# Kernel tuning notes

Hardware: AMD Instinct MI355X
Metric: run time of the kernel (lower is better)

The kernel has to match this reference:

```python
import jax, jax.numpy as jnp
import numpy as np

B, L, D = 2, 4096, 128      # batch, seq_len, d_model
ED = 2 * D                  # d_inner (expand=2) = 256
N = 16                      # d_state
K = 4                       # d_conv
R = (D + 15) // 16          # dt_rank = 8
H = 2 * D                   # mlp hidden = 256


def setup_inputs() -> dict:
    key = jax.random.key(0)
    ks = jax.random.split(key, 20)
    s = 0.05
    inp = {
        "x": jax.random.normal(ks[0], (B, L, D), dtype=jnp.float32),
        # outer block LayerNorm (norm1)
        "norm1_g": jnp.ones((D,), jnp.float32),
        "norm1_b": jnp.zeros((D,), jnp.float32),
        # MambaLayer inner LayerNorm
        "inner_g": jnp.ones((D,), jnp.float32),
        "inner_b": jnp.zeros((D,), jnp.float32),
        # Mamba params
        "in_w": jax.random.normal(ks[1], (2 * ED, D), jnp.float32) * s,      # in_proj (no bias)
        "conv_w": jax.random.normal(ks[2], (ED, 1, K), jnp.float32) * s,     # depthwise conv
        "conv_b": jax.random.normal(ks[3], (ED,), jnp.float32) * s,
        "xproj_w": jax.random.normal(ks[4], (R + 2 * N, ED), jnp.float32) * s,  # x_proj (no bias)
        "dt_w": jax.random.normal(ks[5], (ED, R), jnp.float32) * s,
        "dt_b": jax.random.normal(ks[6], (ED,), jnp.float32) * s,
        "A_log": jnp.tile(jnp.log(jnp.arange(1, N + 1, dtype=jnp.float32)), (ED, 1)),  # [ED,N]
        "Dp": jnp.ones((ED,), jnp.float32),
        "out_w": jax.random.normal(ks[7], (D, ED), jnp.float32) * s,         # out_proj (no bias)
        # MLP
        "fc1_w": jax.random.normal(ks[8], (H, D), jnp.float32) * s,
        "fc1_b": jnp.zeros((H,), jnp.float32),
        "fc2_w": jax.random.normal(ks[9], (D, H), jnp.float32) * s,
        "fc2_b": jnp.zeros((D,), jnp.float32),
    }
    return inp


def _ln(x, g, b, eps=1e-5):
    m = jnp.mean(x, axis=-1, keepdims=True)
    v = jnp.mean((x - m) ** 2, axis=-1, keepdims=True)
    return (x - m) * jax.lax.rsqrt(v + eps) * g + b


def _mamba(x, in_w, conv_w, conv_b, xproj_w, dt_w, dt_b, A_log, Dp, out_w):
    # x: [B, L, D]
    xz = jnp.einsum('bld,ed->ble', x, in_w)          # [B,L,2*ED]
    u, z = jnp.split(xz, 2, axis=-1)                 # each [B,L,ED]
    # causal depthwise conv1d over L
    u_c = jnp.transpose(u, (0, 2, 1))                # [B,ED,L]
    u_c = jax.lax.conv_general_dilated(
        u_c, conv_w, window_strides=(1,), padding=[(K - 1, 0)],
        dimension_numbers=('NCH', 'OIH', 'NCH'), feature_group_count=ED)
    u = jax.nn.silu(jnp.transpose(u_c, (0, 2, 1)) + conv_b)   # [B,L,ED]
    # input-dependent dt, B, C
    dbc = jnp.einsum('ble,re->blr', u, xproj_w)      # [B,L,R+2N]
    dt, Bm, Cm = jnp.split(dbc, [R, R + N], axis=-1)
    delta = jax.nn.softplus(jnp.einsum('blr,er->ble', dt, dt_w) + dt_b)  # [B,L,ED]
    A = -jnp.exp(A_log)                              # [ED,N]
    deltaA = jnp.exp(jnp.einsum('ble,en->blen', delta, A))               # [B,L,ED,N]
    deltaBu = jnp.einsum('ble,bln,ble->blen', delta, Bm, u)              # [B,L,ED,N]
    # selective scan over L
    def step(h, inp):
        dA, dBu, Ct = inp                            # [B,ED,N],[B,ED,N],[B,N]
        h = dA * h + dBu
        y = jnp.einsum('ben,bn->be', h, Ct)
        return h, y
    h0 = jnp.zeros((B, ED, N), u.dtype)
    xs = (jnp.transpose(deltaA, (1, 0, 2, 3)),
          jnp.transpose(deltaBu, (1, 0, 2, 3)),
          jnp.transpose(Cm, (1, 0, 2)))
    _, ys = jax.lax.scan(step, h0, xs)               # [L,B,ED]
    y = jnp.transpose(ys, (1, 0, 2)) + u * Dp        # [B,L,ED]
    y = y * jax.nn.silu(z)
    return jnp.einsum('ble,de->bld', y, out_w)       # [B,L,D]


def reference(x, norm1_g, norm1_b, inner_g, inner_b, in_w, conv_w, conv_b,
              xproj_w, dt_w, dt_b, A_log, Dp, out_w, fc1_w, fc1_b, fc2_w, fc2_b):
    # attn branch: mamba(inner_LN(norm1(x)))
    a = _mamba(_ln(_ln(x, norm1_g, norm1_b), inner_g, inner_b),
               in_w, conv_w, conv_b, xproj_w, dt_w, dt_b, A_log, Dp, out_w)
    x = x + a
    # mlp branch (note: original applies norm1 again to updated x)
    h = _ln(x, norm1_g, norm1_b)
    h = jax.nn.gelu(jnp.einsum('bld,hd->blh', h, fc1_w) + fc1_b, approximate=False)
    h = jnp.einsum('blh,dh->bld', h, fc2_w) + fc2_b
    return x + h
```

## Files before the change

kernel.cpp:

```cpp
#include <hip/hip_runtime.h>
#include <hip/hip_bf16.h>
#include <math.h>

#define BB 2
#define LL 4096
#define DD 128
#define ED 256
#define NN 16
#define KK 4
#define RR 8
#define HH 256
#define NT (BB*LL)
#define NC 128
#define LC 32
#define NCS 256
#define LCS 16

#define LOG2E 1.4426950408889634f

typedef __attribute__((ext_vector_type(8))) short short8;
typedef __attribute__((ext_vector_type(8))) unsigned short ushort8v;
typedef __attribute__((ext_vector_type(4))) float floatx4;

__device__ __forceinline__ unsigned short f2bf(float f) {
  unsigned int b = __builtin_bit_cast(unsigned int, f);
  b += 0x7FFFu + ((b >> 16) & 1u);
  return (unsigned short)(b >> 16);
}

__device__ __forceinline__ float exp2_fast(float x) {
#if __has_builtin(__builtin_amdgcn_exp2f)
  return __builtin_amdgcn_exp2f(x);
#else
  return exp2f(x);
#endif
}

__device__ __forceinline__ ushort8v pack8(const float4& v0, const float4& v1) {
  ushort8v p;
  p[0]=f2bf(v0.x); p[1]=f2bf(v0.y); p[2]=f2bf(v0.z); p[3]=f2bf(v0.w);
  p[4]=f2bf(v1.x); p[5]=f2bf(v1.y); p[6]=f2bf(v1.z); p[7]=f2bf(v1.w);
  return p;
}

__global__ __launch_bounds__(512, 4) void scan1j_k(
    const float* __restrict__ x,
    const float* __restrict__ g1, const float* __restrict__ b1,
    const float* __restrict__ g2, const float* __restrict__ b2,
    const float* __restrict__ in_w,
    const float* __restrict__ cw, const float* __restrict__ cb,
    const float* __restrict__ xpw,
    const float* __restrict__ dtw, const float* __restrict__ dtb,
    const float* __restrict__ A_log,
    float* __restrict__ uc, float* __restrict__ dbc,
    float* __restrict__ delta, float* __restrict__ gate,
    float* __restrict__ cA, float* __restrict__ cH) {
  __shared__ __align__(16) unsigned char SM[51152];
  auto Atile = reinterpret_cast<unsigned short(*)[136]>(SM);
  auto As    = reinterpret_cast<unsigned short(*)[264]>(SM);
  auto Wch   = reinterpret_cast<unsigned short(*)[136]>(SM + 8704);
  auto Bs    = reinterpret_cast<unsigned short(*)[264]>(SM + 8704);
  auto ubuf  = reinterpret_cast<float(*)[65]>(SM + 29824);
  auto sdbc  = reinterpret_cast<float(*)[40]>(SM + 29824);
  auto sus   = reinterpret_cast<float(*)[256]>(SM + 34768);

  const int c2 = blockIdx.x, b = blockIdx.y;
  const int tid = threadIdx.x;
  const int t0 = b*LL + c2*LCS;
  const int wave = tid >> 6, lane = tid & 63;
  const int quad = lane >> 4, l16 = lane & 15;

  {
    const int lr = tid >> 2, lk = (tid & 3) * 32;
    if (lr < 32) {
      if (lr < 19 && !(c2 == 0 && lr < 3)) {
        const float* Ap = x + (size_t)(t0 - 3 + lr)*DD + lk;
        float4 av[8];
        float s = 0.f, sq = 0.f;
        #pragma unroll
        for (int g = 0; g < 8; g++) {
          av[g] = *(const float4*)(Ap + g*4);
          s  += av[g].x + av[g].y + av[g].z + av[g].w;
          sq += av[g].x*av[g].x + av[g].y*av[g].y + av[g].z*av[g].z + av[g].w*av[g].w;
        }
        s += __shfl_xor(s, 1);  s += __shfl_xor(s, 2);
        sq += __shfl_xor(sq, 1); sq += __shfl_xor(sq, 2);
        const float m1 = s * (1.f/128.f);
        const float rs1 = rsqrtf(sq*(1.f/128.f) - m1*m1 + 1e-5f);
        float s2 = 0.f, sq2 = 0.f;
        #pragma unroll
        for (int g = 0; g < 8; g++) {
          const float4 gg = *(const float4*)(g1 + lk + g*4);
          const float4 bb = *(const float4*)(b1 + lk + g*4);
          av[g].x = (av[g].x - m1)*rs1*gg.x + bb.x;
          av[g].y = (av[g].y - m1)*rs1*gg.y + bb.y;
          av[g].z = (av[g].z - m1)*rs1*gg.z + bb.z;
          av[g].w = (av[g].w - m1)*rs1*gg.w + bb.w;
          s2  += av[g].x + av[g].y + av[g].z + av[g].w;
          sq2 += av[g].x*av[g].x + av[g].y*av[g].y + av[g].z*av[g].z + av[g].w*av[g].w;
        }
        s2 += __shfl_xor(s2, 1);  s2 += __shfl_xor(s2, 2);
        sq2 += __shfl_xor(sq2, 1); sq2 += __shfl_xor(sq2, 2);
        const float m2 = s2 * (1.f/128.f);
        const float rs2 = rsqrtf(sq2*(1.f/128.f) - m2*m2 + 1e-5f);
        #pragma unroll
        for (int g = 0; g < 4; g++) {
          const float4 ga = *(const float4*)(g2 + lk + g*8);
          const float4 gb = *(const float4*)(g2 + lk + g*8 + 4);
          const float4 ba = *(const float4*)(b2 + lk + g*8);
          const float4 bbv= *(const float4*)(b2 + lk + g*8 + 4);
          ushort8v pa;
          pa[0] = f2bf((av[2*g].x   - m2)*rs2*ga.x + ba.x);
          pa[1] = f2bf((av[2*g].y   - m2)*rs2*ga.y + ba.y);
          pa[2] = f2bf((av[2*g].z   - m2)*rs2*ga.z + ba.z);
          pa[3] = f2bf((av[2*g].w   - m2)*rs2*ga.w + ba.w);
          pa[4] = f2bf((av[2*g+1].x - m2)*rs2*gb.x + bbv.x);
          pa[5] = f2bf((av[2*g+1].y - m2)*rs2*gb.y + bbv.y);
          pa[6] = f2bf((av[2*g+1].z - m2)*rs2*gb.z + bbv.z);
          pa[7] = f2bf((av[2*g+1].w - m2)*rs2*gb.w + bbv.w);
          *(ushort8v*)&Atile[lr][lk + g*8] = pa;
        }
      } else {
        const ushort8v zz = {};
        #pragma unroll
        for (int g = 0; g < 4; g++) *(ushort8v*)&Atile[lr][lk + g*8] = zz;
      }
    }
  }
  __syncthreads();

  short8 af[2][4];
  #pragma unroll
  for (int mt = 0; mt < 2; mt++)
    #pragma unroll
    for (int ks = 0; ks < 4; ks++)
      af[mt][ks] = *(const short8*)&Atile[mt*16 + l16][ks*32 + quad*8];

  {
    const int wr = tid >> 3;
    const int wseg = (tid & 7) * 16;
    const int mt_w = wave & 1, nt_w = wave >> 1;
    float4 wv[4];
    #pragma unroll
    for (int g = 0; g < 4; g++)
      wv[g] = *(const float4*)(in_w + (size_t)wr*DD + wseg + g*4);
    for (int nc = 0; nc < 8; nc++) {
      *(ushort8v*)&Wch[wr][wseg]     = pack8(wv[0], wv[1]);
      *(ushort8v*)&Wch[wr][wseg + 8] = pack8(wv[2], wv[3]);
      __syncthreads();
      if (nc < 7) {
        const float* wp = in_w + (size_t)((nc+1)*64 + wr)*DD + wseg;
        #pragma unroll
        for (int g = 0; g < 4; g++) wv[g] = *(const float4*)(wp + g*4);
      }
      floatx4 acc = {};
      #pragma unroll
      for (int ks = 0; ks < 4; ks++) {
        short8 bv = *(const short8*)&Wch[nt_w*16 + l16][ks*32 + quad*8];
        acc = __builtin_amdgcn_mfma_f32_16x16x32_bf16(af[mt_w][ks], bv, acc, 0, 0, 0);
      }
      const int coll = nt_w*16 + l16;
      if (nc < 4) {
        #pragma unroll
        for (int rr = 0; rr < 4; rr++) {
          const int m = mt_w*16 + quad*4 + rr;
          if (m < 19) ubuf[m][coll] = acc[rr];
        }
      } else {
        const int gcol = (nc-4)*64 + coll;
        #pragma unroll
        for (int rr = 0; rr < 4; rr++) {
          const int m = mt_w*16 + quad*4 + rr;
          if (m >= 3 && m < 19) {
            const float v = acc[rr];
            gate[(size_t)(t0 + m - 3)*ED + gcol] = v / (1.f + __expf(-v));
          }
        }
      }
      __syncthreads();
      if (nc < 4) {
        const int chl = tid & 63, tg = tid >> 6;
        const int ch = nc*64 + chl;
        const float4 w = *(const float4*)(cw + ch*4);
        const float cbe = cb[ch];
        const int i0 = tg*2;
        float v0 = ubuf[i0][chl], v1 = ubuf[i0+1][chl], v2 = ubuf[i0+2][chl];
        #pragma unroll
        for (int k = 0; k < 2; k++) {
          const float cur = ubuf[i0+3+k][chl];
          const float a = cbe + v0*w.x + v1*w.y + v2*w.z + cur*w.w;
          const float s = a / (1.f + __expf(-a));
          const int i = i0 + k;
          As[i][ch] = f2bf(s);
          sus[i][ch] = s;
          uc[(size_t)(t0+i)*ED + ch] = s;
          v0 = v1; v1 = v2; v2 = cur;
        }
      }
    }
  }
  __syncthreads();

  #pragma unroll
  for (int p = 0; p < 3; p++) {
    const int idx = p*512 + tid;
    if (idx < 1280) {
      const int row = idx >> 5;
      const int col = (idx & 31) * 8;
      const float4 v0 = *(const float4*)(xpw + (size_t)row*ED + col);
      const float4 v1 = *(const float4*)(xpw + (size_t)row*ED + col + 4);
      *(ushort8v*)&Bs[row][col] = pack8(v0, v1);
    }
  }
  __syncthreads();

  if (wave < 3) {
    const int jn = (wave == 2) ? 24 : wave*16;
    floatx4 acc = {};
    #pragma unroll
    for (int ks = 0; ks < 8; ks++) {
      const int ko = ks*32 + quad*8;
      short8 a  = *(const short8*)&As[l16][ko];
      short8 bv = *(const short8*)&Bs[jn + l16][ko];
      acc = __builtin_amdgcn_mfma_f32_16x16x32_bf16(a, bv, acc, 0, 0, 0);
    }
    const int n = jn + l16;
    if (wave < 2 || l16 >= 8) {
      #pragma unroll
      for (int rr = 0; rr < 4; rr++) {
        const int m = quad*4 + rr;
        sdbc[m][n] = acc[rr];
        dbc[(size_t)(t0 + m)*40 + n] = acc[rr];
      }
    }
  }
  __syncthreads();

  {
    const int e = tid >> 1, half = tid & 1;
    const int n0 = half * 8;
    const float4 dw0 = *(const float4*)(dtw + e*RR);
    const float4 dw1 = *(const float4*)(dtw + e*RR + 4);
    const float db = dtb[e];
    const float4 a0 = *(const float4*)(A_log + e*NN + n0);
    const float4 a1 = *(const float4*)(A_log + e*NN + n0 + 4);
    float Aen[8] = {-__expf(a0.x)*LOG2E, -__expf(a0.y)*LOG2E,
                    -__expf(a0.z)*LOG2E, -__expf(a0.w)*LOG2E,
                    -__expf(a1.x)*LOG2E, -__expf(a1.y)*LOG2E,
                    -__expf(a1.z)*LOG2E, -__expf(a1.w)*LOG2E};
    float h[8] = {};
    float sumd = 0.f;
    for (int t = 0; t < LCS; t++) {
      const float4 q0 = *(const float4*)&sdbc[t][0];
      const float4 q1 = *(const float4*)&sdbc[t][4];
      const float aa = db
          + q0.x*dw0.x + q0.y*dw0.y + q0.z*dw0.z + q0.w*dw0.w
          + q1.x*dw1.x + q1.y*dw1.y + q1.z*dw1.z + q1.w*dw1.w;
      const float dv = (aa > 20.f) ? aa : log1pf(__expf(aa));
      if (half == 0) delta[(size_t)(t0+t)*ED + e] = dv;
      const float du = dv * sus[t][e];
      const float4 B0 = *(const float4*)&sdbc[t][RR + n0];
      const float4 B1 = *(const float4*)&sdbc[t][RR + n0 + 4];
      const float Bv[8] = {B0.x,B0.y,B0.z,B0.w,B1.x,B1.y,B1.z,B1.w};
      sumd += dv;
      #pragma unroll
      for (int j = 0; j < 8; j++)
        h[j] = exp2_fast(dv * Aen[j])*h[j] + Bv[j]*du;
    }
    const size_t base = (((size_t)c2*BB + b)*ED + e)*NN + n0;
    *(float4*)(cA + base)     = make_float4(exp2_fast(sumd*Aen[0]), exp2_fast(sumd*Aen[1]),
                                            exp2_fast(sumd*Aen[2]), exp2_fast(sumd*Aen[3]));
    *(float4*)(cA + base + 4) = make_float4(exp2_fast(sumd*Aen[4]), exp2_fast(sumd*Aen[5]),
                                            exp2_fast(sumd*Aen[6]), exp2_fast(sumd*Aen[7]));
    *(float4*)(cH + base)     = make_float4(h[0], h[1], h[2], h[3]);
    *(float4*)(cH + base + 4) = make_float4(h[4], h[5], h[6], h[7]);
  }
}

__global__ __launch_bounds__(256) void scan2p8_k(float* __restrict__ cA,
    const float* __restrict__ cH) {
  const int gt = blockIdx.x*256 + threadIdx.x;
  const int scan = gt >> 3;
  const int seg  = gt & 7;
  const int lane = threadIdx.x & 63;
  const int lb   = lane & ~7;
  const int b = scan >> 12;
  const size_t base = (size_t)b*ED*NN + (scan & 4095);
  const int c0 = seg * 32;

  float ap = 1.f, hs = 0.f;
  for (int g = 0; g < 2; g++) {
    float av[16], hv[16];
    #pragma unroll
    for (int i = 0; i < 16; i++) {
      const size_t idx = (size_t)(c0 + g*16 + i)*(BB*ED*NN) + base;
      av[i] = cA[idx]; hv[i] = cH[idx];
    }
    #pragma unroll
    for (int i = 0; i < 16; i++) {
      hs = av[i]*hs + hv[i];
      ap *= av[i];
    }
  }
  float h = 0.f;
  #pragma unroll
  for (int k = 0; k < 7; k++) {
    const float ak = __shfl(ap, lb + k);
    const float hk = __shfl(hs, lb + k);
    if (seg > k) h = ak*h + hk;
  }
  for (int g = 0; g < 2; g++) {
    float av[16], hv[16];
    #pragma unroll
    for (int i = 0; i < 16; i++) {
      const size_t idx = (size_t)(c0 + g*16 + i)*(BB*ED*NN) + base;
      av[i] = cA[idx]; hv[i] = cH[idx];
    }
    #pragma unroll
    for (int i = 0; i < 16; i++) {
      const size_t idx = (size_t)(c0 + g*16 + i)*(BB*ED*NN) + base;
      cA[idx] = h;
      h = av[i]*h + hv[i];
    }
  }
}

__global__ __launch_bounds__(1024) void tail8_k(
    const float* __restrict__ gate, const float* __restrict__ delta,
    const float* __restrict__ uc, const float* __restrict__ dbc,
    const float* __restrict__ cP, const float* __restrict__ A_log,
    const float* __restrict__ Dpv, const float* __restrict__ x,
    const float* __restrict__ g1, const float* __restrict__ b1,
    const float* __restrict__ out_w, const float* __restrict__ fc1_w,
    const float* __restrict__ fc1_b, const float* __restrict__ fc2_w,
    const float* __restrict__ fc2_b, float* __restrict__ out) {
  __shared__ __align__(16) unsigned short BigW[34816];
  __shared__ __align__(16) unsigned short Au[32][264];
  __shared__ float xs[32][132];
  __shared__ float sbc[32][32];

  const int c = blockIdx.x, b = blockIdx.y;
  const int t0 = b*LL + c*LC;
  const int tid = threadIdx.x;
  const int wave = tid >> 6, lane = tid & 63;
  const int quad = lane >> 4, l16 = lane & 15;

  if (tid < 256) {
    const int row = tid >> 3, c4 = (tid & 7) * 4;
    *(float4*)&sbc[row][c4] = *(const float4*)(dbc + (size_t)(t0 + row)*40 + RR + c4);
  }
  __syncthreads();

  {
    const int r = tid >> 3, k0 = (tid & 7) * 32;
    const float* wp = out_w + (size_t)r*ED + k0;
    #pragma unroll
    for (int g = 0; g < 4; g++) {
      const float4 v0 = *(const float4*)(wp + g*8);
      const float4 v1 = *(const float4*)(wp + g*8 + 4);
      *(ushort8v*)&BigW[(size_t)r*264 + k0 + g*8] = pack8(v0, v1);
    }
  }

  {
    const int e = tid >> 2, q = tid & 3;
    const int n0 = q * 4;
    float Aen[4], h[4];
    {
      const float4 a0 = *(const float4*)(A_log + e*NN + n0);
      Aen[0]=-__expf(a0.x)*LOG2E; Aen[1]=-__expf(a0.y)*LOG2E;
      Aen[2]=-__expf(a0.z)*LOG2E; Aen[3]=-__expf(a0.w)*LOG2E;
      const float4 h0 = *(const float4*)(cP + (((size_t)(2*c)*BB + b)*ED + e)*NN + n0);
      h[0]=h0.x; h[1]=h0.y; h[2]=h0.z; h[3]=h0.w;
    }
    const float Dpe = Dpv[e];
    float pd[8], pu[8], pg[8];
    #pragma unroll
    for (int i = 0; i < 8; i++) {
      pd[i] = delta[(size_t)(t0+i)*ED + e];
      pu[i] = uc[(size_t)(t0+i)*ED + e];
      pg[i] = gate[(size_t)(t0+i)*ED + e];
    }
    for (int g4 = 0; g4 < 4; g4++) {
      float cd[8], cu[8], cg[8];
      #pragma unroll
      for (int i = 0; i < 8; i++) { cd[i]=pd[i]; cu[i]=pu[i]; cg[i]=pg[i]; }
      if (g4 < 3) {
        const int tn = t0 + (g4+1)*8;
        #pragma unroll
        for (int i = 0; i < 8; i++) {
          pd[i] = delta[(size_t)(tn+i)*ED + e];
          pu[i] = uc[(size_t)(tn+i)*ED + e];
          pg[i] = gate[(size_t)(tn+i)*ED + e];
        }
      }
      #pragma unroll
      for (int i = 0; i < 8; i++) {
        const int t = g4*8 + i;
        const float dv = cd[i];
        const float uv = cu[i];
        const float du = dv * uv;
        const float4 B0 = *(const float4*)&sbc[t][n0];
        const float4 C0 = *(const float4*)&sbc[t][16 + n0];
        const float Bv[4] = {B0.x,B0.y,B0.z,B0.w};
        const float Cv[4] = {C0.x,C0.y,C0.z,C0.w};
        float part = 0.f;
        #pragma unroll
        for (int j = 0; j < 4; j++) {
          h[j] = exp2_fast(dv * Aen[j])*h[j] + Bv[j]*du;
          part += h[j]*Cv[j];
        }
        part += __shfl_xor(part, 1);
        part += __shfl_xor(part, 2);
        if (q == 0)
          Au[t][e] = f2bf((part + uv*Dpe) * cg[i]);
      }
    }
  }
  __syncthreads();

  {
    const int mi = (wave & 1) * 16;
    const int wn = (wave >> 1) * 16;
    floatx4 acc = {};
    #pragma unroll
    for (int ks = 0; ks < 8; ks++) {
      const int ko = ks*32 + quad*8;
      short8 a  = *(const short8*)&Au[mi + l16][ko];
      short8 bv = *(const short8*)&BigW[(size_t)(wn + l16)*264 + ko];
      acc = __builtin_amdgcn_mfma_f32_16x16x32_bf16(a, bv, acc, 0, 0, 0);
    }
    const int n = wn + l16;
    #pragma unroll
    for (int r = 0; r < 4; r++) {
      const int m = mi + quad*4 + r;
      xs[m][n] = acc[r] + x[(size_t)(t0 + m)*DD + n];
    }
  }
  __syncthreads();

  if (tid < 512) {
    const int lr = tid >> 4, le = (tid & 15) * 8;
    float vv[8];
    float s = 0.f, sq = 0.f;
    #pragma unroll
    for (int i = 0; i < 8; i++) {
      vv[i] = xs[lr][le + i];
      s += vv[i]; sq += vv[i]*vv[i];
    }
    s += __shfl_xor(s, 1);  s += __shfl_xor(s, 2);
    s += __shfl_xor(s, 4);  s += __shfl_xor(s, 8);
    sq += __shfl_xor(sq, 1); sq += __shfl_xor(sq, 2);
    sq += __shfl_xor(sq, 4); sq += __shfl_xor(sq, 8);
    const float mean = s * (1.f/128.f);
    const float rs = rsqrtf(sq*(1.f/128.f) - mean*mean + 1e-5f);
    ushort8v p;
    #pragma unroll
    for (int i = 0; i < 8; i++)
      p[i] = f2bf((vv[i] - mean)*rs*g1[le + i] + b1[le + i]);
    *(ushort8v*)&Au[lr][le] = p;
  }
  {
    const int r = tid >> 2, k0 = (tid & 3) * 32;
    const float* wp = fc1_w + (size_t)r*DD + k0;
    #pragma unroll
    for (int g = 0; g < 4; g++) {
      const float4 v0 = *(const float4*)(wp + g*8);
      const float4 v1 = *(const float4*)(wp + g*8 + 4);
      *(ushort8v*)&BigW[(size_t)r*136 + k0 + g*8] = pack8(v0, v1);
    }
  }
  __syncthreads();

  {
    const int mi = (wave & 1) * 16;
    const int wn = (wave >> 1) * 32;
    floatx4 acc[2] = {};
    #pragma unroll
    for (int ks = 0; ks < 4; ks++) {
      const int ko = ks*32 + quad*8;
      short8 a  = *(const short8*)&Au[mi + l16][ko];
      short8 b0 = *(const short8*)&BigW[(size_t)(wn +      l16)*136 + ko];
      short8 b1 = *(const short8*)&BigW[(size_t)(wn + 16 + l16)*136 + ko];
      acc[0] = __builtin_amdgcn_mfma_f32_16x16x32_bf16(a, b0, acc[0], 0, 0, 0);
      acc[1] = __builtin_amdgcn_mfma_f32_16x16x32_bf16(a, b1, acc[1], 0, 0, 0);
    }
    __syncthreads();
    #pragma unroll
    for (int f = 0; f < 2; f++) {
      const int n = wn + f*16 + l16;
      const float bn = fc1_b[n];
      #pragma unroll
      for (int r = 0; r < 4; r++) {
        const int m = mi + quad*4 + r;
        float v = acc[f][r] + bn;
        v = 0.5f*v*(1.f + erff(v*0.70710678118f));
        Au[m][n] = f2bf(v);
      }
    }
  }
  {
    const int r = tid >> 3, k0 = (tid & 7) * 32;
    const float* wp = fc2_w + (size_t)r*HH + k0;
    #pragma unroll
    for (int g = 0; g < 4; g++) {
      const float4 v0 = *(const float4*)(wp + g*8);
      const float4 v1 = *(const float4*)(wp + g*8 + 4);
      *(ushort8v*)&BigW[(size_t)r*264 + k0 + g*8] = pack8(v0, v1);
    }
  }
  __syncthreads();

  {
    const int mi = (wave & 1) * 16;
    const int wn = (wave >> 1) * 16;
    floatx4 acc = {};
    #pragma unroll
    for (int ks = 0; ks < 8; ks++) {
      const int ko = ks*32 + quad*8;
      short8 a  = *(const short8*)&Au[mi + l16][ko];
      short8 bv = *(const short8*)&BigW[(size_t)(wn + l16)*264 + ko];
      acc = __builtin_amdgcn_mfma_f32_16x16x32_bf16(a, bv, acc, 0, 0, 0);
    }
    const int n = wn + l16;
    const float bn = fc2_b[n];
    #pragma unroll
    for (int r = 0; r < 4; r++) {
      const int m = mi + quad*4 + r;
      out[(size_t)(t0 + m)*DD + n] = acc[r] + bn + xs[m][n];
    }
  }
}

extern "C" void kernel_launch(void* const* d_in, const int* in_sizes, int n_in,
                              void* d_out, int out_size, void* d_ws, size_t ws_size,
                              hipStream_t stream) {
  const float* x      = (const float*)d_in[0];
  const float* n1g    = (const float*)d_in[1];
  const float* n1b    = (const float*)d_in[2];
  const float* ing    = (const float*)d_in[3];
  const float* inb    = (const float*)d_in[4];
  const float* in_w   = (const float*)d_in[5];
  const float* conv_w = (const float*)d_in[6];
  const float* conv_b = (const float*)d_in[7];
  const float* xproj_w= (const float*)d_in[8];
  const float* dt_w   = (const float*)d_in[9];
  const float* dt_b   = (const float*)d_in[10];
  const float* A_log  = (const float*)d_in[11];
  const float* Dpv    = (const float*)d_in[12];
  const float* out_w  = (const float*)d_in[13];
  const float* fc1_w  = (const float*)d_in[14];
  const float* fc1_b  = (const float*)d_in[15];
  const float* fc2_w  = (const float*)d_in[16];
  const float* fc2_b  = (const float*)d_in[17];
  float* out = (float*)d_out;

  float* ws    = (float*)d_ws;
  float* uc    = ws;
  float* dbc   = uc    + (size_t)NT*ED;
  float* delta = dbc   + (size_t)NT*40;
  float* gate  = delta + (size_t)NT*ED;
  float* cA    = gate  + (size_t)NT*ED;
  float* cH    = cA    + (size_t)NCS*BB*ED*NN;

  scan1j_k<<<dim3(NCS, BB), 512, 0, stream>>>(x, n1g, n1b, ing, inb, in_w,
                                              conv_w, conv_b, xproj_w, dt_w, dt_b,
                                              A_log, uc, dbc, delta, gate, cA, cH);
  scan2p8_k<<<(8*BB*ED*NN)/256, 256, 0, stream>>>(cA, cH);
  tail8_k<<<dim3(NC, BB), 1024, 0, stream>>>(gate, delta, uc, dbc, cA, A_log, Dpv,
                                             x, n1g, n1b, out_w, fc1_w, fc1_b,
                                             fc2_w, fc2_b, out);
}
```

Before: 189.0 us.

## Pre-convert weights to bf16 once and read MFMA operands directly from global

```diff
diff --git a/kernel.cpp b/kernel.cpp
--- a/kernel.cpp
+++ b/kernel.cpp
@@ -43,26 +43,46 @@
   return p;
 }
 
-__global__ __launch_bounds__(512, 4) void scan1j_k(
+#define S_IN  65536
+#define S_XP  10240
+#define S_OUT 32768
+#define S_F1  32768
+#define S_F2  32768
+__global__ __launch_bounds__(256) void prep_k(
+    const float* __restrict__ in_w, const float* __restrict__ xpw,
+    const float* __restrict__ out_w, const float* __restrict__ fc1_w,
+    const float* __restrict__ fc2_w, unsigned short* __restrict__ wb) {
+  const int o = (blockIdx.x*256 + threadIdx.x) * 8;
+  const float* src;
+  int off;
+  if (o < S_IN)                          { src = in_w;  off = o; }
+  else if (o < S_IN+S_XP)                { src = xpw;   off = o - S_IN; }
+  else if (o < S_IN+S_XP+S_OUT)          { src = out_w; off = o - S_IN - S_XP; }
+  else if (o < S_IN+S_XP+S_OUT+S_F1)     { src = fc1_w; off = o - S_IN - S_XP - S_OUT; }
+  else                                   { src = fc2_w; off = o - S_IN - S_XP - S_OUT - S_F1; }
+  const float4 v0 = *(const float4*)(src + off);
+  const float4 v1 = *(const float4*)(src + off + 4);
+  *(ushort8v*)(wb + o) = pack8(v0, v1);
+}
+
+__global__ __launch_bounds__(512, 4) void scan1m_k(
     const float* __restrict__ x,
     const float* __restrict__ g1, const float* __restrict__ b1,
     const float* __restrict__ g2, const float* __restrict__ b2,
-    const float* __restrict__ in_w,
+    const unsigned short* __restrict__ wb_in,
     const float* __restrict__ cw, const float* __restrict__ cb,
-    const float* __restrict__ xpw,
+    const unsigned short* __restrict__ wb_xp,
     const float* __restrict__ dtw, const float* __restrict__ dtb,
     const float* __restrict__ A_log,
     float* __restrict__ uc, float* __restrict__ dbc,
     float* __restrict__ delta, float* __restrict__ gate,
     float* __restrict__ cA, float* __restrict__ cH) {
-  __shared__ __align__(16) unsigned char SM[51152];
+  __shared__ __align__(16) unsigned char SM[44624];
   auto Atile = reinterpret_cast<unsigned short(*)[136]>(SM);
   auto As    = reinterpret_cast<unsigned short(*)[264]>(SM);
-  auto Wch   = reinterpret_cast<unsigned short(*)[136]>(SM + 8704);
-  auto Bs    = reinterpret_cast<unsigned short(*)[264]>(SM + 8704);
-  auto ubuf  = reinterpret_cast<float(*)[65]>(SM + 29824);
-  auto sdbc  = reinterpret_cast<float(*)[40]>(SM + 29824);
-  auto sus   = reinterpret_cast<float(*)[256]>(SM + 34768);
+  auto ubuf  = reinterpret_cast<float(*)[257]>(SM + 8704);
+  auto sdbc  = reinterpret_cast<float(*)[40]>(SM + 8704);
+  auto sus   = reinterpret_cast<float(*)[256]>(SM + 28240);
 
   const int c2 = blockIdx.x, b = blockIdx.y;
   const int tid = threadIdx.x;
@@ -129,87 +149,58 @@
   }
   __syncthreads();
 
-  short8 af[2][4];
-  #pragma unroll
-  for (int mt = 0; mt < 2; mt++)
+  {
+    const int mt = wave >> 2;
+    short8 af[4];
     #pragma unroll
     for (int ks = 0; ks < 4; ks++)
-      af[mt][ks] = *(const short8*)&Atile[mt*16 + l16][ks*32 + quad*8];
-
-  {
-    const int wr = tid >> 3;
-    const int wseg = (tid & 7) * 16;
-    const int mt_w = wave & 1, nt_w = wave >> 1;
-    float4 wv[4];
-    #pragma unroll
-    for (int g = 0; g < 4; g++)
-      wv[g] = *(const float4*)(in_w + (size_t)wr*DD + wseg + g*4);
-    for (int nc = 0; nc < 8; nc++) {
-      *(ushort8v*)&Wch[wr][wseg]     = pack8(wv[0], wv[1]);
-      *(ushort8v*)&Wch[wr][wseg + 8] = pack8(wv[2], wv[3]);
-      __syncthreads();
-      if (nc < 7) {
-        const float* wp = in_w + (size_t)((nc+1)*64 + wr)*DD + wseg;
-        #pragma unroll
-        for (int g = 0; g < 4; g++) wv[g] = *(const float4*)(wp + g*4);
-      }
+      af[ks] = *(const short8*)&Atile[mt*16 + l16][ks*32 + quad*8];
+    #pragma unroll
+    for (int j = 0; j < 8; j++) {
+      const int ncol = ((wave & 3)*8 + j) * 16;
       floatx4 acc = {};
       #pragma unroll
       for (int ks = 0; ks < 4; ks++) {
-        short8 bv = *(const short8*)&Wch[nt_w*16 + l16][ks*32 + quad*8];
-        acc = __builtin_amdgcn_mfma_f32_16x16x32_bf16(af[mt_w][ks], bv, acc, 0, 0, 0);
-      }
-      const int coll = nt_w*16 + l16;
-      if (nc < 4) {
+        short8 bv = *(const short8*)(wb_in + (size_t)(ncol + l16)*DD + ks*32 + quad*8);
+        acc = __builtin_amdgcn_mfma_f32_16x16x32_bf16(af[ks], bv, acc, 0, 0, 0);
+      }
+      const int coll = ncol + l16;
+      if (ncol < 256) {
         #pragma unroll
         for (int rr = 0; rr < 4; rr++) {
-          const int m = mt_w*16 + quad*4 + rr;
+          const int m = mt*16 + quad*4 + rr;
           if (m < 19) ubuf[m][coll] = acc[rr];
         }
       } else {
-        const int gcol = (nc-4)*64 + coll;
         #pragma unroll
         for (int rr = 0; rr < 4; rr++) {
-          const int m = mt_w*16 + quad*4 + rr;
+          const int m = mt*16 + quad*4 + rr;
           if (m >= 3 && m < 19) {
             const float v = acc[rr];
-            gate[(size_t)(t0 + m - 3)*ED + gcol] = v / (1.f + __expf(-v));
+            gate[(size_t)(t0 + m - 3)*ED + coll - 256] = v / (1.f + __expf(-v));
           }
         }
       }
-      __syncthreads();
-      if (nc < 4) {
-        const int chl = tid & 63, tg = tid >> 6;
-        const int ch = nc*64 + chl;
-        const float4 w = *(const float4*)(cw + ch*4);
-        const float cbe = cb[ch];
-        const int i0 = tg*2;
-        float v0 = ubuf[i0][chl], v1 = ubuf[i0+1][chl], v2 = ubuf[i0+2][chl];
-        #pragma unroll
-        for (int k = 0; k < 2; k++) {
-          const float cur = ubuf[i0+3+k][chl];
-          const float a = cbe + v0*w.x + v1*w.y + v2*w.z + cur*w.w;
-          const float s = a / (1.f + __expf(-a));
-          const int i = i0 + k;
-          As[i][ch] = f2bf(s);
-          sus[i][ch] = s;
-          uc[(size_t)(t0+i)*ED + ch] = s;
-          v0 = v1; v1 = v2; v2 = cur;
-        }
-      }
-    }
-  }
-  __syncthreads();
-
-  #pragma unroll
-  for (int p = 0; p < 3; p++) {
-    const int idx = p*512 + tid;
-    if (idx < 1280) {
-      const int row = idx >> 5;
-      const int col = (idx & 31) * 8;
-      const float4 v0 = *(const float4*)(xpw + (size_t)row*ED + col);
-      const float4 v1 = *(const float4*)(xpw + (size_t)row*ED + col + 4);
-      *(ushort8v*)&Bs[row][col] = pack8(v0, v1);
+    }
+  }
+  __syncthreads();
+
+  {
+    const int ch = tid & 255, tg = tid >> 8;
+    const int i0 = tg * 8;
+    const float4 w = *(const float4*)(cw + ch*4);
+    const float cbe = cb[ch];
+    float v0 = ubuf[i0][ch], v1 = ubuf[i0+1][ch], v2 = ubuf[i0+2][ch];
+    #pragma unroll
+    for (int k = 0; k < 8; k++) {
+      const float cur = ubuf[i0+3+k][ch];
+      const float a = cbe + v0*w.x + v1*w.y + v2*w.z + cur*w.w;
+      const float s = a / (1.f + __expf(-a));
+      const int i = i0 + k;
+      As[i][ch] = f2bf(s);
+      sus[i][ch] = s;
+      uc[(size_t)(t0+i)*ED + ch] = s;
+      v0 = v1; v1 = v2; v2 = cur;
     }
   }
   __syncthreads();
@@ -221,7 +212,7 @@
     for (int ks = 0; ks < 8; ks++) {
       const int ko = ks*32 + quad*8;
       short8 a  = *(const short8*)&As[l16][ko];
-      short8 bv = *(const short8*)&Bs[jn + l16][ko];
+      short8 bv = *(const short8*)(wb_xp + (size_t)(jn + l16)*ED + ko);
       acc = __builtin_amdgcn_mfma_f32_16x16x32_bf16(a, bv, acc, 0, 0, 0);
     }
     const int n = jn + l16;
@@ -325,16 +316,17 @@
   }
 }
 
-__global__ __launch_bounds__(1024) void tail8_k(
+__global__ __launch_bounds__(1024) void tail9_k(
     const float* __restrict__ gate, const float* __restrict__ delta,
     const float* __restrict__ uc, const float* __restrict__ dbc,
     const float* __restrict__ cP, const float* __restrict__ A_log,
     const float* __restrict__ Dpv, const float* __restrict__ x,
     const float* __restrict__ g1, const float* __restrict__ b1,
-    const float* __restrict__ out_w, const float* __restrict__ fc1_w,
-    const float* __restrict__ fc1_b, const float* __restrict__ fc2_w,
-    const float* __restrict__ fc2_b, float* __restrict__ out) {
-  __shared__ __align__(16) unsigned short BigW[34816];
+    const unsigned short* __restrict__ wb_out,
+    const unsigned short* __restrict__ wb_f1,
+    const unsigned short* __restrict__ wb_f2,
+    const float* __restrict__ fc1_b, const float* __restrict__ fc2_b,
+    float* __restrict__ out) {
   __shared__ __align__(16) unsigned short Au[32][264];
   __shared__ float xs[32][132];
   __shared__ float sbc[32][32];
@@ -350,17 +342,6 @@
     *(float4*)&sbc[row][c4] = *(const float4*)(dbc + (size_t)(t0 + row)*40 + RR + c4);
   }
   __syncthreads();
-
-  {
-    const int r = tid >> 3, k0 = (tid & 7) * 32;
-    const float* wp = out_w + (size_t)r*ED + k0;
-    #pragma unroll
-    for (int g = 0; g < 4; g++) {
-      const float4 v0 = *(const float4*)(wp + g*8);
-      const float4 v1 = *(const float4*)(wp + g*8 + 4);
-      *(ushort8v*)&BigW[(size_t)r*264 + k0 + g*8] = pack8(v0, v1);
-    }
-  }
 
   {
     const int e = tid >> 2, q = tid & 3;
@@ -427,7 +408,7 @@
     for (int ks = 0; ks < 8; ks++) {
       const int ko = ks*32 + quad*8;
       short8 a  = *(const short8*)&Au[mi + l16][ko];
-      short8 bv = *(const short8*)&BigW[(size_t)(wn + l16)*264 + ko];
+      short8 bv = *(const short8*)(wb_out + (size_t)(wn + l16)*ED + ko);
       acc = __builtin_amdgcn_mfma_f32_16x16x32_bf16(a, bv, acc, 0, 0, 0);
     }
     const int n = wn + l16;
@@ -460,16 +441,6 @@
       p[i] = f2bf((vv[i] - mean)*rs*g1[le + i] + b1[le + i]);
     *(ushort8v*)&Au[lr][le] = p;
   }
-  {
-    const int r = tid >> 2, k0 = (tid & 3) * 32;
-    const float* wp = fc1_w + (size_t)r*DD + k0;
-    #pragma unroll
-    for (int g = 0; g < 4; g++) {
-      const float4 v0 = *(const float4*)(wp + g*8);
-      const float4 v1 = *(const float4*)(wp + g*8 + 4);
-      *(ushort8v*)&BigW[(size_t)r*136 + k0 + g*8] = pack8(v0, v1);
-    }
-  }
   __syncthreads();
 
   {
@@ -480,10 +451,10 @@
     for (int ks = 0; ks < 4; ks++) {
       const int ko = ks*32 + quad*8;
       short8 a  = *(const short8*)&Au[mi + l16][ko];
-      short8 b0 = *(const short8*)&BigW[(size_t)(wn +      l16)*136 + ko];
-      short8 b1 = *(const short8*)&BigW[(size_t)(wn + 16 + l16)*136 + ko];
+      short8 b0 = *(const short8*)(wb_f1 + (size_t)(wn +      l16)*DD + ko);
+      short8 b1v= *(const short8*)(wb_f1 + (size_t)(wn + 16 + l16)*DD + ko);
       acc[0] = __builtin_amdgcn_mfma_f32_16x16x32_bf16(a, b0, acc[0], 0, 0, 0);
-      acc[1] = __builtin_amdgcn_mfma_f32_16x16x32_bf16(a, b1, acc[1], 0, 0, 0);
+      acc[1] = __builtin_amdgcn_mfma_f32_16x16x32_bf16(a, b1v, acc[1], 0, 0, 0);
     }
     __syncthreads();
     #pragma unroll
@@ -499,16 +470,6 @@
       }
     }
   }
-  {
-    const int r = tid >> 3, k0 = (tid & 7) * 32;
-    const float* wp = fc2_w + (size_t)r*HH + k0;
-    #pragma unroll
-    for (int g = 0; g < 4; g++) {
-      const float4 v0 = *(const float4*)(wp + g*8);
-      const float4 v1 = *(const float4*)(wp + g*8 + 4);
-      *(ushort8v*)&BigW[(size_t)r*264 + k0 + g*8] = pack8(v0, v1);
-    }
-  }
   __syncthreads();
 
   {
@@ -519,7 +480,7 @@
     for (int ks = 0; ks < 8; ks++) {
       const int ko = ks*32 + quad*8;
       short8 a  = *(const short8*)&Au[mi + l16][ko];
-      short8 bv = *(const short8*)&BigW[(size_t)(wn + l16)*264 + ko];
+      short8 bv = *(const short8*)(wb_f2 + (size_t)(wn + l16)*HH + ko);
       acc = __builtin_amdgcn_mfma_f32_16x16x32_bf16(a, bv, acc, 0, 0, 0);
     }
     const int n = wn + l16;
@@ -562,12 +523,20 @@
   float* gate  = delta + (size_t)NT*ED;
   float* cA    = gate  + (size_t)NT*ED;
   float* cH    = cA    + (size_t)NCS*BB*ED*NN;
-
-  scan1j_k<<<dim3(NCS, BB), 512, 0, stream>>>(x, n1g, n1b, ing, inb, in_w,
-                                              conv_w, conv_b, xproj_w, dt_w, dt_b,
+  unsigned short* wb = (unsigned short*)(cH + (size_t)NCS*BB*ED*NN);
+  unsigned short* wb_in  = wb;
+  unsigned short* wb_xp  = wb_in  + S_IN;
+  unsigned short* wb_out = wb_xp  + S_XP;
+  unsigned short* wb_f1  = wb_out + S_OUT;
+  unsigned short* wb_f2  = wb_f1  + S_F1;
+
+  prep_k<<<(S_IN+S_XP+S_OUT+S_F1+S_F2)/(256*8), 256, 0, stream>>>(
+      in_w, xproj_w, out_w, fc1_w, fc2_w, wb);
+  scan1m_k<<<dim3(NCS, BB), 512, 0, stream>>>(x, n1g, n1b, ing, inb, wb_in,
+                                              conv_w, conv_b, wb_xp, dt_w, dt_b,
                                               A_log, uc, dbc, delta, gate, cA, cH);
   scan2p8_k<<<(8*BB*ED*NN)/256, 256, 0, stream>>>(cA, cH);
-  tail8_k<<<dim3(NC, BB), 1024, 0, stream>>>(gate, delta, uc, dbc, cA, A_log, Dpv,
-                                             x, n1g, n1b, out_w, fc1_w, fc1_b,
-                                             fc2_w, fc2_b, out);
-}
+  tail9_k<<<dim3(NC, BB), 1024, 0, stream>>>(gate, delta, uc, dbc, cA, A_log, Dpv,
+                                             x, n1g, n1b, wb_out, wb_f1, wb_f2,
+                                             fc1_b, fc2_b, out);
+}
```

Result: faster. 173.3 us (-8.3%).
